# Performance work log

Hardware: AMD Instinct MI355X
Metric: run time of the kernel (lower is better)

## Reference

```python
import jax, jax.numpy as jnp
import numpy as np

EMBED_DIM = 1024
NUM_HEADS = 16
HEAD_DIM = EMBED_DIM // NUM_HEADS


def setup_inputs() -> dict:
    key = jax.random.key(0)
    ks = jax.random.split(key, 9)
    B, S, E, hd = 2, 2048, EMBED_DIM, HEAD_DIM
    s_e = 1.0 / np.sqrt(E)
    return {
        "x": jax.random.normal(ks[0], (B, S, E), dtype=jnp.float32),
        "wq": jax.random.uniform(ks[1], (E, E), jnp.float32, -s_e, s_e),
        "bq": jax.random.uniform(ks[2], (E,), jnp.float32, -s_e, s_e),
        "wk": jax.random.uniform(ks[3], (E, hd), jnp.float32, -s_e, s_e),
        "bk": jax.random.uniform(ks[4], (hd,), jnp.float32, -s_e, s_e),
        "wv": jax.random.uniform(ks[5], (E, hd), jnp.float32, -s_e, s_e),
        "bv": jax.random.uniform(ks[6], (hd,), jnp.float32, -s_e, s_e),
        "wo": jax.random.uniform(ks[7], (E, E), jnp.float32, -s_e, s_e),
        "bo": jax.random.uniform(ks[8], (E,), jnp.float32, -s_e, s_e),
    }


def reference(x, wq, bq, wk, bk, wv, bv, wo, bo):
    B, S, E = x.shape
    H, hd = NUM_HEADS, HEAD_DIM
    # projections
    q = (x @ wq + bq).reshape(B, S, H, hd)          # [B,S,H,hd]
    k = x @ wk + bk                                  # [B,S,hd] shared across heads
    v = x @ wv + bv                                  # [B,S,hd]
    scale = 1.0 / np.sqrt(hd).astype(np.float32)
    # scores: [B,H,S_q,S_k]
    scores = jnp.einsum('bqhd,bkd->bhqk', q, k) * scale
    attn = jax.nn.softmax(scores, axis=-1)
    out = jnp.einsum('bhqk,bkd->bqhd', attn, v).reshape(B, S, E)
    return out @ wo + bo
```

## Files before the change

kernel.cpp:

```cpp
#include <hip/hip_runtime.h>
#include <stdint.h>

#define SLEN 2048
#define EDIM 1024
#define NH 16
#define HD 64
#define QLD 1152
#define NSPLIT 4

typedef unsigned short u16;
typedef short bf8 __attribute__((ext_vector_type(8)));
typedef float f4 __attribute__((ext_vector_type(4)));
typedef float f16f __attribute__((ext_vector_type(16)));
typedef int v2i __attribute__((ext_vector_type(2)));
typedef bf8 bf8_a __attribute__((may_alias));
typedef uint2 uint2_a __attribute__((may_alias));
typedef uint4 uint4_a __attribute__((may_alias));

__device__ __forceinline__ float bf2f(u16 u) {
  union { unsigned u; float f; } c; c.u = ((unsigned)u) << 16; return c.f;
}
__device__ __forceinline__ u16 f2bf(float x) {
  union { __bf16 h; u16 u; } c; c.h = (__bf16)x; return c.u;
}
__device__ __forceinline__ unsigned pk2bf(float a, float b) {
  union { __bf16 h[2]; unsigned u; } c;
  c.h[0] = (__bf16)a; c.h[1] = (__bf16)b;
  return c.u;
}
__device__ __forceinline__ void async_cp16(u16* lds, const u16* g) {
  __builtin_amdgcn_global_load_lds((__attribute__((address_space(1))) void*)g,
                                   (__attribute__((address_space(3))) void*)lds,
                                   16, 0, 0);
}

__device__ __forceinline__ void tcvt_tile(const float* src, int srcLd,
                                          u16* dst, int dstLd, int r0, int c0) {
  __shared__ u16 tile[64][65];
  const int t = threadIdx.x;
#pragma unroll
  for (int i = 0; i < 16; ++i) {
    int e = i * 256 + t, rr = e >> 6, cc = e & 63;
    tile[rr][cc] = f2bf(src[(size_t)(r0 + rr) * srcLd + c0 + cc]);
  }
  __syncthreads();
#pragma unroll
  for (int i = 0; i < 16; ++i) {
    int e = i * 256 + t, j = e >> 6, ii = e & 63;
    dst[(size_t)(c0 + j) * dstLd + r0 + ii] = tile[ii][j];
  }
}

__global__ void prep_w(const float* wq, const float* wk, const float* wv,
                       const float* wo, const float* bq, const float* bk,
                       const float* bv, const float* bo, const float* x,
                       u16* wT, u16* woT, float* bQKV, float* bOut, u16* xbf) {
  const int yy = blockIdx.y;
  if (yy < 16) tcvt_tile(wq, 1024, wT, 1024, blockIdx.x * 64, yy * 64);
  else if (yy < 32) tcvt_tile(wo, 1024, woT, 1024, blockIdx.x * 64, (yy - 16) * 64);
  else if (yy == 32) tcvt_tile(wk, 64, wT + (size_t)1024 * 1024, 1024, blockIdx.x * 64, 0);
  else if (yy == 33) tcvt_tile(wv, 64, wT + (size_t)1088 * 1024, 1024, blockIdx.x * 64, 0);
  else if (yy == 34) {
    int i = blockIdx.x * 256 + threadIdx.x;
    if (i < 1024) bQKV[i] = bq[i];
    else if (i < 1088) bQKV[i] = bk[i - 1024];
    else if (i < 1152) bQKV[i] = bv[i - 1088];
    int j = i - 1152;
    if (j >= 0 && j < 1024) bOut[j] = bo[j];
  } else {
    const int blk = (yy - 35) * 16 + blockIdx.x, t = threadIdx.x;
#pragma unroll
    for (int i = 0; i < 8; ++i) {
      int idx = blk * 16384 + i * 2048 + t * 8;
      u16 tmp[8];
#pragma unroll
      for (int j = 0; j < 8; ++j) tmp[j] = f2bf(x[idx + j]);
      *(uint4_a*)&xbf[idx] = *(const uint4_a*)tmp;
    }
  }
}

__global__ __launch_bounds__(256) void gemm_bt_bias(
    const u16* __restrict__ A, const u16* __restrict__ Bt,
    const float* __restrict__ bias, void* __restrict__ C, int K, int ldc,
    int ofp32, u16* __restrict__ vtb) {
  __shared__ __align__(16) u16 As[2][64 * 64];
  __shared__ __align__(16) u16 Bs[2][128 * 64];
  const int tn0 = blockIdx.x * 128, tm0 = blockIdx.y * 64;
  const int tid = threadIdx.x, wave = tid >> 6, lane = tid & 63;
  const int quad = lane >> 4, l16 = lane & 15;
  const int wm = wave & 1, wn = wave >> 1;

  f4 acc[2][4];
#pragma unroll
  for (int i = 0; i < 2; ++i)
#pragma unroll
    for (int j = 0; j < 4; ++j) acc[i][j] = f4{0.f, 0.f, 0.f, 0.f};

  int aslot[2], bslot[4]; size_t aoff[2], boff[4];
#pragma unroll
  for (int i = 0; i < 2; ++i) {
    int s = i * 256 + tid, m = s >> 3, kc = s & 7, c = (kc - m) & 7;
    aslot[i] = s; aoff[i] = (size_t)(tm0 + m) * K + c * 8;
  }
#pragma unroll
  for (int i = 0; i < 4; ++i) {
    int s = i * 256 + tid, n = s >> 3, kc = s & 7, c = (kc - n) & 7;
    bslot[i] = s; boff[i] = (size_t)(tn0 + n) * K + c * 8;
  }
  int ard[2][2], brd[4][2];
#pragma unroll
  for (int mi = 0; mi < 2; ++mi) {
    int m = wm * 32 + mi * 16 + l16;
#pragma unroll
    for (int kk = 0; kk < 2; ++kk)
      ard[mi][kk] = (m * 8 + (((kk * 4 + quad) + m) & 7)) * 8;
  }
#pragma unroll
  for (int ni = 0; ni < 4; ++ni) {
    int n = wn * 64 + ni * 16 + l16;
#pragma unroll
    for (int kk = 0; kk < 2; ++kk)
      brd[ni][kk] = (n * 8 + (((kk * 4 + quad) + n) & 7)) * 8;
  }

  auto stage = [&](int it, int bsel) {
    const size_t kb = (size_t)it * 64;
#pragma unroll
    for (int i = 0; i < 2; ++i)
      async_cp16(&As[bsel][aslot[i] * 8], A + aoff[i] + kb);
#pragma unroll
    for (int i = 0; i < 4; ++i)
      async_cp16(&Bs[bsel][bslot[i] * 8], Bt + boff[i] + kb);
  };

  const int kIt = K >> 6;
  stage(0, 0);
  for (int it = 0; it < kIt; ++it) {
    __syncthreads();
    if (it + 1 < kIt) stage(it + 1, (it + 1) & 1);
    const int bsel = it & 1;
#pragma unroll
    for (int kk = 0; kk < 2; ++kk) {
      bf8 af[2], bfr[4];
#pragma unroll
      for (int mi = 0; mi < 2; ++mi)
        af[mi] = *(const bf8_a*)&As[bsel][ard[mi][kk]];
#pragma unroll
      for (int ni = 0; ni < 4; ++ni)
        bfr[ni] = *(const bf8_a*)&Bs[bsel][brd[ni][kk]];
#pragma unroll
      for (int mi = 0; mi < 2; ++mi)
#pragma unroll
        for (int ni = 0; ni < 4; ++ni)
          acc[mi][ni] = __builtin_amdgcn_mfma_f32_16x16x32_bf16(
              af[mi], bfr[ni], acc[mi][ni], 0, 0, 0);
    }
  }

  float bv[4];
#pragma unroll
  for (int ni = 0; ni < 4; ++ni) bv[ni] = bias[tn0 + wn * 64 + ni * 16 + l16];
#pragma unroll
  for (int mi = 0; mi < 2; ++mi) {
    int row0 = tm0 + wm * 32 + mi * 16 + quad * 4;
#pragma unroll
    for (int ni = 0; ni < 4; ++ni) {
      int col = tn0 + wn * 64 + ni * 16 + l16;
      float vv[4];
#pragma unroll
      for (int r = 0; r < 4; ++r) vv[r] = acc[mi][ni][r] + bv[ni];
      if (ofp32) {
#pragma unroll
        for (int r = 0; r < 4; ++r)
          ((float*)C)[(size_t)(row0 + r) * ldc + col] = vv[r];
      } else {
#pragma unroll
        for (int r = 0; r < 4; ++r)
          ((u16*)C)[(size_t)(row0 + r) * ldc + col] = f2bf(vv[r]);
      }
      if (vtb != nullptr && col >= 1088) {
        int d = col - 1088, bb = row0 >> 11, s0 = row0 & 2047;
        uint2 pk;
        pk.x = pk2bf(vv[0], vv[1]);
        pk.y = pk2bf(vv[2], vv[3]);
        *(uint2_a*)&vtb[(size_t)(bb * 64 + d) * SLEN + s0] = pk;
      }
    }
  }
}

__global__ __launch_bounds__(256, 5) void attn_kernel(
    const u16* __restrict__ qkv, const u16* __restrict__ vT,
    u16* __restrict__ Opart, float* __restrict__ lpart) {
  __shared__ __align__(16) u16 Kf[2][4096];
  __shared__ __align__(16) u16 Vf[2][4096];
  const int qt = blockIdx.x, bh = blockIdx.y, ks = blockIdx.z;
  const int b = bh >> 4, h = bh & 15;
  const int tid = threadIdx.x, wave = tid >> 6, lane = tid & 63;
  const int l31 = lane & 31, hi = lane >> 5, r16l = lane & 15;
  const int base_k = (l31 >> 4) * 64 + hi * 16 + r16l;

  u16* Kflat = &Kf[0][0];
#pragma unroll
  for (int i = 0; i < 4; ++i) {
    int d = i * 256 + tid;
    int kk = d >> 9, g = (d >> 6) & 7, qd = (d >> 4) & 3, r16 = d & 15;
    async_cp16(&Kflat[d * 8],
               qkv + (size_t)(b * SLEN + qt * 128 + g * 16 + r16) * QLD +
                   h * HD + (kk * 4 + qd) * 8);
  }
  __syncthreads();
  bf8 bq[4];
#pragma unroll
  for (int kk2 = 0; kk2 < 4; ++kk2) {
    int c = base_k + wave * 128 + (kk2 >> 1) * 512 + (kk2 & 1) * 32;
    bq[kk2] = *(const bf8_a*)&Kflat[c * 8];
  }
  __syncthreads();

  const int kbase = ks * (SLEN / NSPLIT);
  auto stage = [&](int hh, int bsel) {
#pragma unroll
    for (int i = 0; i < 2; ++i) {
      int d = i * 256 + tid;
      int kk = d >> 8, k8 = (d >> 6) & 3, qd = (d >> 4) & 3, r16 = d & 15;
      async_cp16(&Kf[bsel][d * 8],
                 qkv + (size_t)(b * SLEN + kbase + hh * 64 + k8 * 16 + r16) * QLD +
                     EDIM + (kk * 4 + qd) * 8);
    }
#pragma unroll
    for (int i = 0; i < 2; ++i) {
      int d = i * 256 + tid;
      int k4 = d >> 8, ni = (d >> 6) & 3, qd = (d >> 4) & 3, r16 = d & 15;
      async_cp16(&Vf[bsel][d * 8],
                 vT + (size_t)(b * 64 + ni * 16 + r16) * SLEN + kbase + hh * 64 +
                     (k4 * 4 + qd) * 8);
    }
  };
  stage(0, 0);

  f16f acc_o[2];
#pragma unroll
  for (int i = 0; i < 2; ++i)
#pragma unroll
    for (int r = 0; r < 16; ++r) acc_o[i][r] = 0.f;
  float lr = 0.f;
  const float C1 = 0.125f * 1.44269504089f;

  const int NHALF = SLEN / NSPLIT / 64;
  for (int hh = 0; hh < NHALF; ++hh) {
    __syncthreads();
    if (hh < NHALF - 1) stage(hh + 1, (hh + 1) & 1);
    const int bsel = hh & 1;
    const u16* kf = &Kf[bsel][0];
    const u16* vf = &Vf[bsel][0];

#pragma unroll
    for (int j32 = 0; j32 < 2; ++j32) {
      f16f st;
#pragma unroll
      for (int r = 0; r < 16; ++r) st[r] = 0.f;
      __builtin_amdgcn_s_setprio(1);
#pragma unroll
      for (int kk2 = 0; kk2 < 4; ++kk2) {
        bf8 ak = *(const bf8_a*)
            &kf[(base_k + (kk2 >> 1) * 256 + j32 * 128 + (kk2 & 1) * 32) * 8];
        st = __builtin_amdgcn_mfma_f32_32x32x16_bf16(ak, bq[kk2], st, 0, 0, 0);
      }
      __builtin_amdgcn_s_setprio(0);

      float pe[16];
#pragma unroll
      for (int r = 0; r < 16; ++r) {
        pe[r] = __builtin_amdgcn_exp2f(st[r] * C1);
        lr += pe[r];
      }
      int a0 = (int)pk2bf(pe[0], pe[1]),   b0 = (int)pk2bf(pe[4], pe[5]);
      int a1 = (int)pk2bf(pe[2], pe[3]),   b1 = (int)pk2bf(pe[6], pe[7]);
      int a2 = (int)pk2bf(pe[8], pe[9]),   b2 = (int)pk2bf(pe[12], pe[13]);
      int a3 = (int)pk2bf(pe[10], pe[11]), b3 = (int)pk2bf(pe[14], pe[15]);
      v2i s0 = __builtin_amdgcn_permlane32_swap(a0, b0, false, false);
      v2i s1 = __builtin_amdgcn_permlane32_swap(a1, b1, false, false);
      v2i s2 = __builtin_amdgcn_permlane32_swap(a2, b2, false, false);
      v2i s3 = __builtin_amdgcn_permlane32_swap(a3, b3, false, false);
      union { int i[4]; bf8 v; } up0, up1;
      up0.i[0] = s0[0]; up0.i[1] = s1[0]; up0.i[2] = s0[1]; up0.i[3] = s1[1];
      up1.i[0] = s2[0]; up1.i[1] = s3[0]; up1.i[2] = s2[1]; up1.i[3] = s3[1];

      __builtin_amdgcn_s_setprio(1);
#pragma unroll
      for (int ks2 = 0; ks2 < 2; ++ks2) {
        bf8 pa = ks2 ? up1.v : up0.v;
#pragma unroll
        for (int ni2 = 0; ni2 < 2; ++ni2) {
          bf8 bv = *(const bf8_a*)
              &vf[(base_k + j32 * 256 + ni2 * 128 + ks2 * 32) * 8];
          acc_o[ni2] = __builtin_amdgcn_mfma_f32_32x32x16_bf16(
              pa, bv, acc_o[ni2], 0, 0, 0);
        }
      }
      __builtin_amdgcn_s_setprio(0);
    }
  }

  const size_t pbase = (size_t)((ks * 32 + bh) * 16 + qt) * 128;
  float s = lr + __shfl_xor(lr, 32, 64);
  if (lane < 32) lpart[pbase + wave * 32 + lane] = s;
#pragma unroll
  for (int ni2 = 0; ni2 < 2; ++ni2)
#pragma unroll
    for (int r = 0; r < 16; ++r) {
      int q = (r & 3) + 8 * (r >> 2) + 4 * hi;
      Opart[(pbase + wave * 32 + q) * 64 + ni2 * 32 + l31] =
          f2bf(acc_o[ni2][r]);
    }
}

__global__ __launch_bounds__(256) void reduce_o(const u16* __restrict__ Op,
                                                const float* __restrict__ lp,
                                                u16* __restrict__ aob) {
  const int qt = blockIdx.x, bh = blockIdx.y, b = bh >> 4, h = bh & 15;
  const int t = threadIdx.x, r = t >> 1, dh = (t & 1) * 32;
  size_t p[NSPLIT];
#pragma unroll
  for (int i = 0; i < NSPLIT; ++i)
    p[i] = (size_t)((i * 32 + bh) * 16 + qt) * 128;
  float lsum = 0.f;
#pragma unroll
  for (int i = 0; i < NSPLIT; ++i) lsum += lp[p[i] + r];
  const float inv = 1.f / lsum;
  u16* dst = aob + (size_t)(b * SLEN + qt * 128 + r) * EDIM + h * HD + dh;
#pragma unroll
  for (int c = 0; c < 4; ++c) {
    float accv[8] = {0.f, 0.f, 0.f, 0.f, 0.f, 0.f, 0.f, 0.f};
#pragma unroll
    for (int i = 0; i < NSPLIT; ++i) {
      uint4 a = *(const uint4_a*)(Op + (p[i] + r) * 64 + dh + c * 8);
      const u16* pa = (const u16*)&a;
#pragma unroll
      for (int j = 0; j < 8; ++j) accv[j] += bf2f(pa[j]);
    }
    u16 outv[8];
#pragma unroll
    for (int j = 0; j < 8; ++j) outv[j] = f2bf(accv[j] * inv);
    *(uint4_a*)(dst + c * 8) = *(const uint4_a*)outv;
  }
}

extern "C" void kernel_launch(void* const* d_in, const int* in_sizes, int n_in,
                              void* d_out, int out_size, void* d_ws, size_t ws_size,
                              hipStream_t stream) {
  const float* x  = (const float*)d_in[0];
  const float* wq = (const float*)d_in[1];
  const float* bq = (const float*)d_in[2];
  const float* wk = (const float*)d_in[3];
  const float* bk = (const float*)d_in[4];
  const float* wv = (const float*)d_in[5];
  const float* bv = (const float*)d_in[6];
  const float* wo = (const float*)d_in[7];
  const float* bo = (const float*)d_in[8];

  char* ws = (char*)d_ws;
  size_t off = 0;
  auto carve = [&](size_t bytes) {
    void* p = ws + off;
    off = (off + bytes + 255) & ~(size_t)255;
    return p;
  };
  u16* wT      = (u16*)carve((size_t)1152 * 1024 * 2);
  u16* woT     = (u16*)carve((size_t)1024 * 1024 * 2);
  float* bQKV  = (float*)carve(1152 * 4);
  float* bOut  = (float*)carve(1024 * 4);
  u16* xbf     = (u16*)carve((size_t)4096 * EDIM * 2);
  u16* qkvb    = (u16*)carve((size_t)4096 * QLD * 2);
  u16* vTb     = (u16*)carve((size_t)2 * 64 * SLEN * 2);
  u16* Opart   = (u16*)carve((size_t)NSPLIT * 32 * 16 * 128 * 64 * 2);
  float* lpart = (float*)carve((size_t)NSPLIT * 32 * 16 * 128 * 4);
  u16* aob     = (u16*)carve((size_t)4096 * EDIM * 2);

  prep_w<<<dim3(16, 51), 256, 0, stream>>>(wq, wk, wv, wo, bq, bk, bv, bo, x,
                                           wT, woT, bQKV, bOut, xbf);

  gemm_bt_bias<<<dim3(9, 64), 256, 0, stream>>>(xbf, wT, bQKV, qkvb, 1024, QLD,
                                                0, vTb);

  attn_kernel<<<dim3(16, 32, NSPLIT), 256, 0, stream>>>(qkvb, vTb, Opart, lpart);
  reduce_o<<<dim3(16, 32), 256, 0, stream>>>(Opart, lpart, aob);

  gemm_bt_bias<<<dim3(8, 64), 256, 0, stream>>>(aob, woT, bOut, d_out, 1024,
                                                1024, 1, nullptr);
}
```

Before: 189.5 us.

## Use 128x128 single-buffered GEMM tiles and halve attention K-splits

```diff
diff --git a/kernel.cpp b/kernel.cpp
--- a/kernel.cpp
+++ b/kernel.cpp
@@ -6,7 +6,7 @@
 #define NH 16
 #define HD 64
 #define QLD 1152
-#define NSPLIT 4
+#define NSPLIT 2
 
 typedef unsigned short u16;
 typedef short bf8 __attribute__((ext_vector_type(8)));
@@ -84,34 +84,31 @@
     const u16* __restrict__ A, const u16* __restrict__ Bt,
     const float* __restrict__ bias, void* __restrict__ C, int K, int ldc,
     int ofp32, u16* __restrict__ vtb) {
-  __shared__ __align__(16) u16 As[2][64 * 64];
-  __shared__ __align__(16) u16 Bs[2][128 * 64];
-  const int tn0 = blockIdx.x * 128, tm0 = blockIdx.y * 64;
+  __shared__ __align__(16) u16 As[128 * 64];
+  __shared__ __align__(16) u16 Bs[128 * 64];
+  const int tn0 = blockIdx.x * 128, tm0 = blockIdx.y * 128;
   const int tid = threadIdx.x, wave = tid >> 6, lane = tid & 63;
   const int quad = lane >> 4, l16 = lane & 15;
   const int wm = wave & 1, wn = wave >> 1;
 
-  f4 acc[2][4];
-#pragma unroll
-  for (int i = 0; i < 2; ++i)
+  f4 acc[4][4];
+#pragma unroll
+  for (int i = 0; i < 4; ++i)
 #pragma unroll
     for (int j = 0; j < 4; ++j) acc[i][j] = f4{0.f, 0.f, 0.f, 0.f};
 
-  int aslot[2], bslot[4]; size_t aoff[2], boff[4];
-#pragma unroll
-  for (int i = 0; i < 2; ++i) {
+  int aslot[4]; size_t aoff[4], boff[4];
+#pragma unroll
+  for (int i = 0; i < 4; ++i) {
     int s = i * 256 + tid, m = s >> 3, kc = s & 7, c = (kc - m) & 7;
-    aslot[i] = s; aoff[i] = (size_t)(tm0 + m) * K + c * 8;
-  }
-#pragma unroll
-  for (int i = 0; i < 4; ++i) {
-    int s = i * 256 + tid, n = s >> 3, kc = s & 7, c = (kc - n) & 7;
-    bslot[i] = s; boff[i] = (size_t)(tn0 + n) * K + c * 8;
-  }
-  int ard[2][2], brd[4][2];
-#pragma unroll
-  for (int mi = 0; mi < 2; ++mi) {
-    int m = wm * 32 + mi * 16 + l16;
+    aslot[i] = s;
+    aoff[i] = (size_t)(tm0 + m) * K + c * 8;
+    boff[i] = (size_t)(tn0 + m) * K + c * 8;
+  }
+  int ard[4][2], brd[4][2];
+#pragma unroll
+  for (int mi = 0; mi < 4; ++mi) {
+    int m = wm * 64 + mi * 16 + l16;
 #pragma unroll
     for (int kk = 0; kk < 2; ++kk)
       ard[mi][kk] = (m * 8 + (((kk * 4 + quad) + m) & 7)) * 8;
@@ -124,33 +121,24 @@
       brd[ni][kk] = (n * 8 + (((kk * 4 + quad) + n) & 7)) * 8;
   }
 
-  auto stage = [&](int it, int bsel) {
-    const size_t kb = (size_t)it * 64;
-#pragma unroll
-    for (int i = 0; i < 2; ++i)
-      async_cp16(&As[bsel][aslot[i] * 8], A + aoff[i] + kb);
-#pragma unroll
-    for (int i = 0; i < 4; ++i)
-      async_cp16(&Bs[bsel][bslot[i] * 8], Bt + boff[i] + kb);
-  };
-
   const int kIt = K >> 6;
-  stage(0, 0);
   for (int it = 0; it < kIt; ++it) {
     __syncthreads();
-    if (it + 1 < kIt) stage(it + 1, (it + 1) & 1);
-    const int bsel = it & 1;
+    const size_t kb = (size_t)it * 64;
+#pragma unroll
+    for (int i = 0; i < 4; ++i) async_cp16(&As[aslot[i] * 8], A + aoff[i] + kb);
+#pragma unroll
+    for (int i = 0; i < 4; ++i) async_cp16(&Bs[aslot[i] * 8], Bt + boff[i] + kb);
+    __syncthreads();
 #pragma unroll
     for (int kk = 0; kk < 2; ++kk) {
-      bf8 af[2], bfr[4];
-#pragma unroll
-      for (int mi = 0; mi < 2; ++mi)
-        af[mi] = *(const bf8_a*)&As[bsel][ard[mi][kk]];
-#pragma unroll
-      for (int ni = 0; ni < 4; ++ni)
-        bfr[ni] = *(const bf8_a*)&Bs[bsel][brd[ni][kk]];
-#pragma unroll
-      for (int mi = 0; mi < 2; ++mi)
+      bf8 af[4], bfr[4];
+#pragma unroll
+      for (int mi = 0; mi < 4; ++mi) af[mi] = *(const bf8_a*)&As[ard[mi][kk]];
+#pragma unroll
+      for (int ni = 0; ni < 4; ++ni) bfr[ni] = *(const bf8_a*)&Bs[brd[ni][kk]];
+#pragma unroll
+      for (int mi = 0; mi < 4; ++mi)
 #pragma unroll
         for (int ni = 0; ni < 4; ++ni)
           acc[mi][ni] = __builtin_amdgcn_mfma_f32_16x16x32_bf16(
@@ -158,18 +146,18 @@
     }
   }
 
-  float bv[4];
-#pragma unroll
-  for (int ni = 0; ni < 4; ++ni) bv[ni] = bias[tn0 + wn * 64 + ni * 16 + l16];
-#pragma unroll
-  for (int mi = 0; mi < 2; ++mi) {
-    int row0 = tm0 + wm * 32 + mi * 16 + quad * 4;
+  float bv4[4];
+#pragma unroll
+  for (int ni = 0; ni < 4; ++ni) bv4[ni] = bias[tn0 + wn * 64 + ni * 16 + l16];
+#pragma unroll
+  for (int mi = 0; mi < 4; ++mi) {
+    int row0 = tm0 + wm * 64 + mi * 16 + quad * 4;
 #pragma unroll
     for (int ni = 0; ni < 4; ++ni) {
       int col = tn0 + wn * 64 + ni * 16 + l16;
       float vv[4];
 #pragma unroll
-      for (int r = 0; r < 4; ++r) vv[r] = acc[mi][ni][r] + bv[ni];
+      for (int r = 0; r < 4; ++r) vv[r] = acc[mi][ni][r] + bv4[ni];
       if (ofp32) {
 #pragma unroll
         for (int r = 0; r < 4; ++r)
@@ -190,7 +178,7 @@
   }
 }
 
-__global__ __launch_bounds__(256, 5) void attn_kernel(
+__global__ __launch_bounds__(256, 4) void attn_kernel(
     const u16* __restrict__ qkv, const u16* __restrict__ vT,
     u16* __restrict__ Opart, float* __restrict__ lpart) {
   __shared__ __align__(16) u16 Kf[2][4096];
@@ -382,12 +370,12 @@
   prep_w<<<dim3(16, 51), 256, 0, stream>>>(wq, wk, wv, wo, bq, bk, bv, bo, x,
                                            wT, woT, bQKV, bOut, xbf);
 
-  gemm_bt_bias<<<dim3(9, 64), 256, 0, stream>>>(xbf, wT, bQKV, qkvb, 1024, QLD,
+  gemm_bt_bias<<<dim3(9, 32), 256, 0, stream>>>(xbf, wT, bQKV, qkvb, 1024, QLD,
                                                 0, vTb);
 
   attn_kernel<<<dim3(16, 32, NSPLIT), 256, 0, stream>>>(qkvb, vTb, Opart, lpart);
   reduce_o<<<dim3(16, 32), 256, 0, stream>>>(Opart, lpart, aob);
 
-  gemm_bt_bias<<<dim3(8, 64), 256, 0, stream>>>(aob, woT, bOut, d_out, 1024,
+  gemm_bt_bias<<<dim3(8, 32), 256, 0, stream>>>(aob, woT, bOut, d_out, 1024,
                                                 1024, 1, nullptr);
 }
```

After: 192.1 us. Within noise of the previous version (+1.3%).
